# Kernel tuning notes

Hardware: AMD Instinct MI355X
Metric: run time of the kernel (lower is better)

## Reference

```python
import jax, jax.numpy as jnp
import numpy as np

E, H, HID = 1024, 16, 4096
HD = E // H
EPS = 1e-6


def layer_norm(x, gamma, beta):
    mean = x.mean(axis=-1, keepdims=True)
    var = ((x - mean) ** 2).mean(axis=-1, keepdims=True)
    std = jnp.sqrt(var) + EPS  # note: eps added to std, as in the torch source
    return gamma * ((x - mean) / std) + beta


def setup_inputs() -> dict:
    key = jax.random.key(0)
    ks = jax.random.split(key, 12)
    B, S = 4, 2048
    s = lambda n: 1.0 / np.sqrt(n)
    return {
        "x": jax.random.normal(ks[0], (B, S, E), jnp.float32),
        "mask": jnp.zeros((B, S, S), jnp.float32),
        "Wqkv": jax.random.normal(ks[1], (3 * E, E), jnp.float32) * s(E),
        "bqkv": jnp.zeros((3 * E,), jnp.float32),
        "Wo": jax.random.normal(ks[2], (E, E), jnp.float32) * s(E),
        "bo": jnp.zeros((E,), jnp.float32),
        "W1": jax.random.normal(ks[3], (HID, E), jnp.float32) * s(E),
        "b1": jnp.zeros((HID,), jnp.float32),
        "W2": jax.random.normal(ks[4], (E, HID), jnp.float32) * s(HID),
        "b2": jnp.zeros((E,), jnp.float32),
        "gamma1": jnp.ones((E,), jnp.float32),
        "beta1": jnp.zeros((E,), jnp.float32),
        "gamma2": jnp.ones((E,), jnp.float32),
        "beta2": jnp.zeros((E,), jnp.float32),
    }


def reference(x, mask, Wqkv, bqkv, Wo, bo, W1, b1, W2, b2, gamma1, beta1, gamma2, beta2):
    B, S, _ = x.shape
    # --- multi-headed attention ---
    qkv = x @ Wqkv.T + bqkv                       # [B,S,3E]
    qkv = qkv.reshape(B, S, H, 3 * HD).transpose(0, 2, 1, 3)  # [B,H,S,3*hd]
    q, k, v = jnp.split(qkv, 3, axis=-1)          # each [B,H,S,hd]
    scores = jnp.einsum("bhsd,bhtd->bhst", q, k) / np.sqrt(HD)
    att = jax.nn.softmax(scores + mask[:, None, :, :], axis=-1)
    ctx = jnp.einsum("bhst,bhtd->bhsd", att, v)
    ctx = ctx.transpose(0, 2, 1, 3).reshape(B, S, E)
    attn_out = ctx @ Wo.T + bo
    # residual + LayerNorm 1 (dropout is identity in eval / p=0)
    h = layer_norm(attn_out + x, gamma1, beta1)
    # --- feed forward ---
    ff = jax.nn.relu(h @ W1.T + b1) @ W2.T + b2
    # residual + LayerNorm 2
    return layer_norm(ff + h, gamma2, beta2)
```

## Files before the change

kernel.cpp:

```cpp
#include <hip/hip_runtime.h>

typedef unsigned short u16;
typedef float f32x4 __attribute__((ext_vector_type(4)));
typedef __bf16 bf16x8 __attribute__((ext_vector_type(8)));

#define AS1(p) ((const __attribute__((address_space(1))) void*)(p))
#define AS3(p) ((__attribute__((address_space(3))) void*)(p))

#define LOG2E 1.44269504088896f

__device__ __forceinline__ u16 f2bf(float f) {
    return __builtin_bit_cast(u16, (__bf16)f);
}
__device__ __forceinline__ float bf2f(u16 u) {
    return __builtin_bit_cast(float, (unsigned)u << 16);
}

__global__ __launch_bounds__(256) void cast_all_bf16(
    const float* __restrict__ s0, const float* __restrict__ s1,
    const float* __restrict__ s2, const float* __restrict__ s3,
    const float* __restrict__ s4,
    u16* __restrict__ d0, u16* __restrict__ d1, u16* __restrict__ d2,
    u16* __restrict__ d3, u16* __restrict__ d4)
{
    const int n0 = 2097152;
    const int e1 = n0 + 786432;
    const int e2 = e1 + 262144;
    const int e3 = e2 + 1048576;
    const int e4 = e3 + 1048576;
    int stride = gridDim.x * blockDim.x;
    for (int i = blockIdx.x * blockDim.x + threadIdx.x; i < e4; i += stride) {
        const float* src; u16* dst; int li;
        if (i < n0)      { src = s0; dst = d0; li = i; }
        else if (i < e1) { src = s1; dst = d1; li = i - n0; }
        else if (i < e2) { src = s2; dst = d2; li = i - e1; }
        else if (i < e3) { src = s3; dst = d3; li = i - e2; }
        else             { src = s4; dst = d4; li = i - e3; }
        float4 v = ((const float4*)src)[li];
        ushort4 o;
        o.x = f2bf(v.x); o.y = f2bf(v.y); o.z = f2bf(v.z); o.w = f2bf(v.w);
        ((ushort4*)dst)[li] = o;
    }
}

template <int MODE>
__global__ __launch_bounds__(256)
void gemm_bt(const u16* __restrict__ A, const u16* __restrict__ Bt,
             const float* __restrict__ bias, const float* __restrict__ res,
             const u16* __restrict__ resb,
             void* __restrict__ outp, int M, int N, int K,
             u16* __restrict__ qb, u16* __restrict__ kb, u16* __restrict__ vT)
{
    __shared__ u16 As[2][128 * 32];
    __shared__ u16 Bs[2][128 * 32];
    const int tid = threadIdx.x;
    const int m0 = blockIdx.x * 128, n0 = blockIdx.y * 128;
    const int wid = tid >> 6, lane = tid & 63;
    const int wm = (wid >> 1) * 64, wn = (wid & 1) * 64;
    const int lr = lane & 15, lg = lane >> 4;
    f32x4 acc[4][4] = {};

    const int row0 = tid >> 2, cc0 = (tid & 3) * 8;
    const int row1 = row0 + 64;
    const int lo0 = (tid & ~63) * 16;
    const int lo1 = 256 * 16 + lo0;

#define GSTG(buf, k0_) do {                                                    \
    __builtin_amdgcn_global_load_lds(                                          \
        AS1(A + (size_t)(m0 + row0) * K + (k0_) + cc0),                        \
        AS3((char*)As[buf] + lo0), 16, 0, 0);                                  \
    __builtin_amdgcn_global_load_lds(                                          \
        AS1(A + (size_t)(m0 + row1) * K + (k0_) + cc0),                        \
        AS3((char*)As[buf] + lo1), 16, 0, 0);                                  \
    __builtin_amdgcn_global_load_lds(                                          \
        AS1(Bt + (size_t)(n0 + row0) * K + (k0_) + cc0),                       \
        AS3((char*)Bs[buf] + lo0), 16, 0, 0);                                  \
    __builtin_amdgcn_global_load_lds(                                          \
        AS1(Bt + (size_t)(n0 + row1) * K + (k0_) + cc0),                       \
        AS3((char*)Bs[buf] + lo1), 16, 0, 0);                                  \
} while (0)

    GSTG(0, 0);
    __syncthreads();

    const int NT = K >> 5;
    for (int t = 0; t < NT; ++t) {
        const int cur = t & 1;
        if (t + 1 < NT) GSTG(cur ^ 1, (t + 1) << 5);
        bf16x8 af[4];
#pragma unroll
        for (int i = 0; i < 4; ++i)
            af[i] = *(const bf16x8*)&As[cur][(wm + i * 16 + lr) * 32 + lg * 8];
#pragma unroll
        for (int j = 0; j < 4; ++j) {
            bf16x8 bf = *(const bf16x8*)&Bs[cur][(wn + j * 16 + lr) * 32 + lg * 8];
#pragma unroll
            for (int i = 0; i < 4; ++i)
                acc[i][j] = __builtin_amdgcn_mfma_f32_16x16x32_bf16(af[i], bf, acc[i][j], 0, 0, 0);
        }
        __syncthreads();
    }
#undef GSTG

#pragma unroll
    for (int i = 0; i < 4; ++i) {
#pragma unroll
        for (int j = 0; j < 4; ++j) {
            int col = n0 + wn + j * 16 + lr;
            float bv = bias[col];
#pragma unroll
            for (int r = 0; r < 4; ++r) {
                int mr = m0 + wm + i * 16 + lg * 4 + r;
                float v = acc[i][j][r] + bv;
                if (MODE == 0) {
                    int b_ = mr >> 11, s_ = mr & 2047;
                    int h_ = col / 192, rr = col - h_ * 192;
                    int bh = b_ * 16 + h_;
                    if (rr < 64)
                        qb[((size_t)bh * 2048 + s_) * 64 + rr] = f2bf(v * (0.125f * LOG2E));
                    else if (rr < 128)
                        kb[((size_t)bh * 2048 + s_) * 64 + (rr - 64)] = f2bf(v);
                    else
                        vT[((size_t)bh * 64 + (rr - 128)) * 2048 + s_] = f2bf(v);
                } else if (MODE == 1) {
                    ((u16*)outp)[(size_t)mr * N + col] = f2bf(v + res[(size_t)mr * N + col]);
                } else if (MODE == 3) {
                    ((u16*)outp)[(size_t)mr * N + col] = f2bf(v + bf2f(resb[(size_t)mr * N + col]));
                } else {
                    ((u16*)outp)[(size_t)mr * N + col] = f2bf(fmaxf(v, 0.0f));
                }
            }
        }
    }
}

__global__ __launch_bounds__(512)
void attn_fwd(const u16* __restrict__ qb, const u16* __restrict__ kb,
              const u16* __restrict__ vT, const float* __restrict__ mask,
              u16* __restrict__ ctx)
{
    __shared__ u16 Ks[2][64 * 64];
    __shared__ u16 Vs[2][64 * 64];
    __shared__ u16 Plds[8 * 16 * 68];
    const int tid = threadIdx.x;
    const int wid = tid >> 6, lane = tid & 63;
    const int lr = lane & 15, lg = lane >> 4;
    const int id = blockIdx.x;
    const int job = (id & 7) * 128 + (id >> 3);
    const int qt = job & 15, h = (job >> 4) & 15, b = job >> 8;
    const int bh = b * 16 + h;
    const int q0 = qt * 128 + wid * 16;
    u16* pl = &Plds[wid * 16 * 68];

    const size_t kbase = (size_t)bh * 2048 * 64;
    const size_t vbase = (size_t)bh * 64 * 2048;

    const int cr = tid >> 3, ck = tid & 7;
    const int sk = ck ^ (cr & 7);
    const int lo = (tid & ~63) * 16;

    bf16x8 qf[2];
#pragma unroll
    for (int ks = 0; ks < 2; ++ks)
        qf[ks] = *(const bf16x8*)(qb + ((size_t)bh * 2048 + q0 + lr) * 64 + ks * 32 + lg * 8);

    f32x4 octx[4] = {};
    float lsum[4] = {};
    const size_t mbase = ((size_t)b * 2048 + q0) * 2048;

    {
        __builtin_amdgcn_global_load_lds(AS1(kb + kbase + (size_t)cr * 64 + sk * 8),
                                         AS3((char*)Ks[0] + lo), 16, 0, 0);
        __builtin_amdgcn_global_load_lds(AS1(vT + vbase + (size_t)cr * 2048 + sk * 8),
                                         AS3((char*)Vs[0] + lo), 16, 0, 0);
    }

    for (int it = 0; it < 32; ++it) {
        const int t0 = it * 64;
        const int cur = it & 1;
        __syncthreads();
        if (it < 31) {
            const int tn = t0 + 64;
            __builtin_amdgcn_global_load_lds(AS1(kb + kbase + (size_t)(tn + cr) * 64 + sk * 8),
                                             AS3((char*)Ks[cur ^ 1] + lo), 16, 0, 0);
            __builtin_amdgcn_global_load_lds(AS1(vT + vbase + (size_t)cr * 2048 + tn + sk * 8),
                                             AS3((char*)Vs[cur ^ 1] + lo), 16, 0, 0);
        }

        float mv[4][4];
#pragma unroll
        for (int j = 0; j < 4; ++j)
#pragma unroll
            for (int r = 0; r < 4; ++r)
                mv[j][r] = mask[mbase + (size_t)(lg * 4 + r) * 2048 + t0 + j * 16 + lr];

        f32x4 sc[4];
#pragma unroll
        for (int j = 0; j < 4; ++j) {
            f32x4 s = {0.f, 0.f, 0.f, 0.f};
#pragma unroll
            for (int ks = 0; ks < 2; ++ks) {
                const int R = j * 16 + lr;
                const int off = R * 128 + ((ks * 64 + lg * 16) ^ ((R & 7) * 16));
                bf16x8 kf = *(const bf16x8*)((const char*)Ks[cur] + off);
                s = __builtin_amdgcn_mfma_f32_16x16x32_bf16(qf[ks], kf, s, 0, 0, 0);
            }
            sc[j] = s;
        }

#pragma unroll
        for (int j = 0; j < 4; ++j) {
#pragma unroll
            for (int r = 0; r < 4; ++r) {
                float p = __builtin_amdgcn_exp2f(fmaf(mv[j][r], LOG2E, sc[j][r]) - 24.0f);
                sc[j][r] = p;
                lsum[r] += p;
            }
        }
#pragma unroll
        for (int j = 0; j < 4; ++j)
#pragma unroll
            for (int r = 0; r < 4; ++r)
                pl[(lg * 4 + r) * 68 + j * 16 + lr] = f2bf(sc[j][r]);

#pragma unroll
        for (int ks = 0; ks < 2; ++ks) {
            bf16x8 pa = *(const bf16x8*)&pl[lr * 68 + ks * 32 + lg * 8];
#pragma unroll
            for (int dj = 0; dj < 4; ++dj) {
                const int R = dj * 16 + lr;
                const int off = R * 128 + ((ks * 64 + lg * 16) ^ ((R & 7) * 16));
                bf16x8 vf = *(const bf16x8*)((const char*)Vs[cur] + off);
                octx[dj] = __builtin_amdgcn_mfma_f32_16x16x32_bf16(pa, vf, octx[dj], 0, 0, 0);
            }
        }
    }

#pragma unroll
    for (int r = 0; r < 4; ++r)
#pragma unroll
        for (int o = 1; o < 16; o <<= 1) lsum[r] += __shfl_xor(lsum[r], o);

#pragma unroll
    for (int dj = 0; dj < 4; ++dj)
#pragma unroll
        for (int r = 0; r < 4; ++r) {
            float o = octx[dj][r] / lsum[r];
            ctx[((size_t)b * 2048 + q0 + lg * 4 + r) * 1024 + h * 64 + dj * 16 + lr] = f2bf(o);
        }
}

__global__ __launch_bounds__(256)
void ln_fwd(const u16* __restrict__ in, const float* __restrict__ gamma,
            const float* __restrict__ beta, float* __restrict__ out32,
            u16* __restrict__ outbf)
{
    __shared__ float red[4], red2[4];
    const int tid = threadIdx.x;
    const size_t row = blockIdx.x;
    ushort4 raw = ((const ushort4*)(in + row * 1024))[tid];
    float vx = bf2f(raw.x), vy = bf2f(raw.y), vz = bf2f(raw.z), vw = bf2f(raw.w);
    float s  = vx + vy + vz + vw;
    float s2 = vx * vx + vy * vy + vz * vz + vw * vw;
#pragma unroll
    for (int o = 32; o; o >>= 1) {
        s  += __shfl_xor(s, o);
        s2 += __shfl_xor(s2, o);
    }
    if ((tid & 63) == 0) { red[tid >> 6] = s; red2[tid >> 6] = s2; }
    __syncthreads();
    float mean = (red[0] + red[1] + red[2] + red[3]) * (1.0f / 1024.0f);
    float ex2  = (red2[0] + red2[1] + red2[2] + red2[3]) * (1.0f / 1024.0f);
    float var  = ex2 - mean * mean;
    float inv = 1.0f / (sqrtf(var) + 1e-6f);
    float dx = vx - mean, dy = vy - mean, dz = vz - mean, dw = vw - mean;
    float4 g = ((const float4*)gamma)[tid];
    float4 bb = ((const float4*)beta)[tid];
    float4 o;
    o.x = g.x * dx * inv + bb.x;
    o.y = g.y * dy * inv + bb.y;
    o.z = g.z * dz * inv + bb.z;
    o.w = g.w * dw * inv + bb.w;
    if (out32) ((float4*)(out32 + row * 1024))[tid] = o;
    if (outbf) {
        ushort4 ob;
        ob.x = f2bf(o.x); ob.y = f2bf(o.y); ob.z = f2bf(o.z); ob.w = f2bf(o.w);
        ((ushort4*)(outbf + row * 1024))[tid] = ob;
    }
}

extern "C" void kernel_launch(void* const* d_in, const int* in_sizes, int n_in,
                              void* d_out, int out_size, void* d_ws, size_t ws_size,
                              hipStream_t stream)
{
    (void)in_sizes; (void)n_in; (void)out_size; (void)ws_size;
    const float* x    = (const float*)d_in[0];
    const float* mask = (const float*)d_in[1];
    const float* Wqkv = (const float*)d_in[2];
    const float* bqkv = (const float*)d_in[3];
    const float* Wo   = (const float*)d_in[4];
    const float* bo   = (const float*)d_in[5];
    const float* W1   = (const float*)d_in[6];
    const float* b1   = (const float*)d_in[7];
    const float* W2   = (const float*)d_in[8];
    const float* b2   = (const float*)d_in[9];
    const float* g1   = (const float*)d_in[10];
    const float* be1  = (const float*)d_in[11];
    const float* g2   = (const float*)d_in[12];
    const float* be2  = (const float*)d_in[13];

    char* w = (char*)d_ws;
    u16* x_bf    = (u16*)w;  w += (size_t)8192 * 1024 * 2;
    u16* Wqkv_bf = (u16*)w;  w += (size_t)3072 * 1024 * 2;
    u16* Wo_bf   = (u16*)w;  w += (size_t)1024 * 1024 * 2;
    u16* W1_bf   = (u16*)w;  w += (size_t)4096 * 1024 * 2;
    u16* W2_bf   = (u16*)w;  w += (size_t)1024 * 4096 * 2;
    u16* qbuf    = (u16*)w;  w += (size_t)8192 * 1024 * 2;
    u16* kbuf    = (u16*)w;  w += (size_t)8192 * 1024 * 2;
    u16* vTbuf   = (u16*)w;  w += (size_t)8192 * 1024 * 2;
    u16* ctxbuf  = (u16*)w;  w += (size_t)8192 * 1024 * 2;
    u16* hb_wo   = (u16*)w;  w += (size_t)8192 * 1024 * 2;
    u16* hbf     = (u16*)w;  w += (size_t)8192 * 1024 * 2;
    u16* hb_w2   = (u16*)w;  w += (size_t)8192 * 1024 * 2;
    u16* ff1     = (u16*)w;  w += (size_t)8192 * 4096 * 2;

    cast_all_bf16<<<2048, 256, 0, stream>>>(x, Wqkv, Wo, W1, W2,
                                            x_bf, Wqkv_bf, Wo_bf, W1_bf, W2_bf);

    gemm_bt<0><<<dim3(64, 24), 256, 0, stream>>>(x_bf, Wqkv_bf, bqkv, nullptr, nullptr, nullptr,
                                                 8192, 3072, 1024, qbuf, kbuf, vTbuf);
    attn_fwd<<<1024, 512, 0, stream>>>(qbuf, kbuf, vTbuf, mask, ctxbuf);
    gemm_bt<3><<<dim3(64, 8), 256, 0, stream>>>(ctxbuf, Wo_bf, bo, nullptr, x_bf, hb_wo,
                                                8192, 1024, 1024, nullptr, nullptr, nullptr);
    ln_fwd<<<8192, 256, 0, stream>>>(hb_wo, g1, be1, nullptr, hbf);
    gemm_bt<2><<<dim3(64, 32), 256, 0, stream>>>(hbf, W1_bf, b1, nullptr, nullptr, ff1,
                                                 8192, 4096, 1024, nullptr, nullptr, nullptr);
    gemm_bt<3><<<dim3(64, 8), 256, 0, stream>>>(ff1, W2_bf, b2, nullptr, hbf, hb_w2,
                                                8192, 1024, 4096, nullptr, nullptr, nullptr);
    ln_fwd<<<8192, 256, 0, stream>>>(hb_w2, g2, be2, (float*)d_out, nullptr);
}
```

Baseline: 498.2 us.

## Keep attention probabilities in registers via transposed QK MFMA and permlane swaps

Swaps the MFMA operands so the score tile comes out transposed, with each lane owning a query row. The softmax probabilities are then packed to bf16 and rearranged into the PV A-operand layout with v_permlane32/16_swap. This removes the per-iteration LDS round trip for P and the shared buffer it used. Mask loads become one float4 per tile along the row, and the row-sum reduction shrinks to two shuffles. The cost is correctness risk in the hand-written lane permutation, which depends on gfx950-specific instructions.

```diff
diff --git a/kernel.cpp b/kernel.cpp
--- a/kernel.cpp
+++ b/kernel.cpp
@@ -3,6 +3,7 @@
 typedef unsigned short u16;
 typedef float f32x4 __attribute__((ext_vector_type(4)));
 typedef __bf16 bf16x8 __attribute__((ext_vector_type(8)));
+typedef unsigned uint4v __attribute__((ext_vector_type(4)));
 
 #define AS1(p) ((const __attribute__((address_space(1))) void*)(p))
 #define AS3(p) ((__attribute__((address_space(3))) void*)(p))
@@ -141,7 +142,6 @@
 {
     __shared__ u16 Ks[2][64 * 64];
     __shared__ u16 Vs[2][64 * 64];
-    __shared__ u16 Plds[8 * 16 * 68];
     const int tid = threadIdx.x;
     const int wid = tid >> 6, lane = tid & 63;
     const int lr = lane & 15, lg = lane >> 4;
@@ -150,7 +150,6 @@
     const int qt = job & 15, h = (job >> 4) & 15, b = job >> 8;
     const int bh = b * 16 + h;
     const int q0 = qt * 128 + wid * 16;
-    u16* pl = &Plds[wid * 16 * 68];
 
     const size_t kbase = (size_t)bh * 2048 * 64;
     const size_t vbase = (size_t)bh * 64 * 2048;
@@ -165,8 +164,8 @@
         qf[ks] = *(const bf16x8*)(qb + ((size_t)bh * 2048 + q0 + lr) * 64 + ks * 32 + lg * 8);
 
     f32x4 octx[4] = {};
-    float lsum[4] = {};
-    const size_t mbase = ((size_t)b * 2048 + q0) * 2048;
+    float lsum = 0.0f;
+    const size_t mrow = ((size_t)b * 2048 + q0 + lr) * 2048;
 
     {
         __builtin_amdgcn_global_load_lds(AS1(kb + kbase + (size_t)cr * 64 + sk * 8),
@@ -187,12 +186,10 @@
                                              AS3((char*)Vs[cur ^ 1] + lo), 16, 0, 0);
         }
 
-        float mv[4][4];
+        float4 mv[4];
 #pragma unroll
         for (int j = 0; j < 4; ++j)
-#pragma unroll
-            for (int r = 0; r < 4; ++r)
-                mv[j][r] = mask[mbase + (size_t)(lg * 4 + r) * 2048 + t0 + j * 16 + lr];
+            mv[j] = *(const float4*)(mask + mrow + t0 + j * 16 + lg * 4);
 
         f32x4 sc[4];
 #pragma unroll
@@ -203,7 +200,7 @@
                 const int R = j * 16 + lr;
                 const int off = R * 128 + ((ks * 64 + lg * 16) ^ ((R & 7) * 16));
                 bf16x8 kf = *(const bf16x8*)((const char*)Ks[cur] + off);
-                s = __builtin_amdgcn_mfma_f32_16x16x32_bf16(qf[ks], kf, s, 0, 0, 0);
+                s = __builtin_amdgcn_mfma_f32_16x16x32_bf16(kf, qf[ks], s, 0, 0, 0);
             }
             sc[j] = s;
         }
@@ -212,40 +209,54 @@
         for (int j = 0; j < 4; ++j) {
 #pragma unroll
             for (int r = 0; r < 4; ++r) {
-                float p = __builtin_amdgcn_exp2f(fmaf(mv[j][r], LOG2E, sc[j][r]) - 24.0f);
+                float m = (r == 0) ? mv[j].x : (r == 1) ? mv[j].y : (r == 2) ? mv[j].z : mv[j].w;
+                float p = __builtin_amdgcn_exp2f(fmaf(m, LOG2E, sc[j][r]) - 24.0f);
                 sc[j][r] = p;
-                lsum[r] += p;
+                lsum += p;
             }
         }
-#pragma unroll
-        for (int j = 0; j < 4; ++j)
-#pragma unroll
-            for (int r = 0; r < 4; ++r)
-                pl[(lg * 4 + r) * 68 + j * 16 + lr] = f2bf(sc[j][r]);
-
+
+        bf16x8 pa[2];
 #pragma unroll
         for (int ks = 0; ks < 2; ++ks) {
-            bf16x8 pa = *(const bf16x8*)&pl[lr * 68 + ks * 32 + lg * 8];
+            const int j0 = ks * 2, j1 = ks * 2 + 1;
+            unsigned a0, a1, b0, b1;
+            asm("v_cvt_pk_bf16_f32 %0, %1, %2" : "=v"(a0) : "v"(sc[j0][0]), "v"(sc[j0][1]));
+            asm("v_cvt_pk_bf16_f32 %0, %1, %2" : "=v"(b0) : "v"(sc[j0][2]), "v"(sc[j0][3]));
+            asm("v_cvt_pk_bf16_f32 %0, %1, %2" : "=v"(a1) : "v"(sc[j1][0]), "v"(sc[j1][1]));
+            asm("v_cvt_pk_bf16_f32 %0, %1, %2" : "=v"(b1) : "v"(sc[j1][2]), "v"(sc[j1][3]));
+            asm("v_permlane32_swap_b32 %0, %1" : "+v"(a0), "+v"(a1));
+            asm("v_permlane32_swap_b32 %0, %1" : "+v"(b0), "+v"(b1));
+            asm("v_permlane16_swap_b32 %0, %1" : "+v"(a0), "+v"(a1));
+            asm("v_permlane16_swap_b32 %0, %1" : "+v"(b0), "+v"(b1));
+            uint4v pw = {a0, b0, a1, b1};
+            pa[ks] = __builtin_bit_cast(bf16x8, pw);
+        }
+
+#pragma unroll
+        for (int ks = 0; ks < 2; ++ks) {
 #pragma unroll
             for (int dj = 0; dj < 4; ++dj) {
                 const int R = dj * 16 + lr;
                 const int off = R * 128 + ((ks * 64 + lg * 16) ^ ((R & 7) * 16));
                 bf16x8 vf = *(const bf16x8*)((const char*)Vs[cur] + off);
-                octx[dj] = __builtin_amdgcn_mfma_f32_16x16x32_bf16(pa, vf, octx[dj], 0, 0, 0);
+                octx[dj] = __builtin_amdgcn_mfma_f32_16x16x32_bf16(pa[ks], vf, octx[dj], 0, 0, 0);
             }
         }
     }
 
+    lsum += __shfl_xor(lsum, 16);
+    lsum += __shfl_xor(lsum, 32);
+    float lq[4];
 #pragma unroll
     for (int r = 0; r < 4; ++r)
-#pragma unroll
-        for (int o = 1; o < 16; o <<= 1) lsum[r] += __shfl_xor(lsum[r], o);
+        lq[r] = __shfl(lsum, lg * 4 + r);
 
 #pragma unroll
     for (int dj = 0; dj < 4; ++dj)
 #pragma unroll
         for (int r = 0; r < 4; ++r) {
-            float o = octx[dj][r] / lsum[r];
+            float o = octx[dj][r] / lq[r];
             ctx[((size_t)b * 2048 + q0 + lg * 4 + r) * 1024 + h * 64 + dj * 16 + lr] = f2bf(o);
         }
 }
```

After: 531.2 us. +6.6%, slower.
